# Optimization experiments

Measured on AMD Instinct MI355X. Metric: run time of the kernel, lower is better.

## Reference

```python
import jax, jax.numpy as jnp
from jax import lax
import numpy as np

# inferred ssconv semantics (custom CUDA kernel not in source):
#  - input x: (B, H, W, Cin) channels-last, Cin = per-pixel channel count
#  - in_index: (B, H, W) in [0, IN_GROUPS): routes each input pixel's Cin channels
#    to the corresponding slice of the weight's input-channel dim (gather/scatter MoE-style dispatch)
#  - weight: (OUT_GROUPS*Cout, IN_GROUPS*Cin, kh, kw), bias: (OUT_GROUPS*Cout,)
#  - per output pixel, one out-group is selected (maxout over groups); the kernel
#    returns both the selected Cout channels and the winning group index (out_index)

IN_GROUPS = 4
OUT_GROUPS = 4
STRIDE = 1  # pad = stride//2 in the wrapper; output (H-1)//s+1 == SAME padding


def setup_inputs() -> dict:
    key = jax.random.key(0)
    k1, k2, k3, k4 = jax.random.split(key, 4)
    x = jax.random.normal(k1, (8, 256, 256, 16), dtype=jnp.float32)
    in_index = jax.random.randint(k2, (8, 256, 256), 0, IN_GROUPS, dtype=jnp.int32)
    weight = jax.random.normal(k3, (64, 64, 3, 3), dtype=jnp.float32) * 0.05
    bias = jax.random.normal(k4, (64,), dtype=jnp.float32) * 0.05
    return {"x": x, "in_index": in_index, "weight": weight, "bias": bias}


def reference(x, in_index, weight, bias):
    B, H, W, Cin = x.shape
    OC, IC, kh, kw = weight.shape  # OC = OUT_GROUPS*Cout, IC = IN_GROUPS*Cin
    Cout = OC // OUT_GROUPS

    # dispatch: scatter each pixel's channels into its in-group slice (rest zero)
    onehot = jax.nn.one_hot(in_index, IN_GROUPS, dtype=x.dtype)          # (B,H,W,G)
    x_full = (onehot[..., :, None] * x[..., None, :]).reshape(B, H, W, IN_GROUPS * Cin)

    # dense conv over the dispatched tensor == per-pixel gathered group weights
    w_hwio = jnp.transpose(weight, (2, 3, 1, 0))  # (kh,kw,IC,OC)
    out = lax.conv_general_dilated(
        x_full, w_hwio, window_strides=(STRIDE, STRIDE), padding="SAME",
        dimension_numbers=("NHWC", "HWIO", "NHWC"))
    out = out + bias  # (B,H',W',OC)

    Bo, Ho, Wo, _ = out.shape
    out_g = out.reshape(Bo, Ho, Wo, OUT_GROUPS, Cout)
    scores = out_g.max(axis=-1)                    # (B,H',W',G) per-group response
    out_index = jnp.argmax(scores, axis=-1)        # winning out-group per pixel
    sel = jnp.take_along_axis(out_g, out_index[..., None, None], axis=3)
    sel = jnp.squeeze(sel, axis=3)                 # (B,H',W',Cout)
    return sel, out_index.astype(jnp.int32)
```

## Files before the change

### kernel.cpp

```cpp
#include <hip/hip_runtime.h>

#define H 256
#define W 256
#define BATCH 8
#define CIN 16
#define TW 32
#define TH 4
#define HWC (TW + 2)
#define HHC (TH + 2)
#define NHALO (HWC * HHC)
#define FIX_CAP 16384
#define GAP_TAU 1e-3f

typedef __attribute__((ext_vector_type(8))) short short8;
typedef __attribute__((ext_vector_type(8))) _Float16 half8;
typedef __attribute__((ext_vector_type(4))) float f32x4;

union S8H8 { short8 s; half8 h; };
__device__ __forceinline__ half8 as_h8(short8 s) { S8H8 u; u.s = s; return u.h; }
union HU { _Float16 h; unsigned short u; };
__device__ __forceinline__ unsigned short f2h_bits(float f) { HU u; u.h = (_Float16)f; return u.u; }
__device__ __forceinline__ float h2f(unsigned short b) { HU u; u.u = b; return (float)u.h; }

__device__ __forceinline__ float4 add4(float4 a, float4 b) {
    return make_float4(a.x + b.x, a.y + b.y, a.z + b.z, a.w + b.w);
}
__device__ __forceinline__ float max4(float4 a) {
    return fmaxf(fmaxf(a.x, a.y), fmaxf(a.z, a.w));
}

__global__ void wprep_kernel(const float* __restrict__ w, unsigned short* __restrict__ wt) {
    int i = blockIdx.x * 256 + threadIdx.x;
    if (i >= 73728) return;
    int k   = i & 63;
    int n   = (i >> 6) & 63;
    int sel = (i >> 12) & 1;
    int tap = i >> 13;
    float v = w[(n * 64 + k) * 9 + tap] * 64.0f;
    unsigned short hb = f2h_bits(v);
    unsigned short ob = sel ? f2h_bits((v - h2f(hb)) * 2048.0f) : hb;
    wt[(((tap * 2 + sel) * 64) + n) * 64 + k] = ob;
}

#define CVT(F, VH, VL, J) { unsigned short hb_ = f2h_bits(F); \
    VH[J] = (short)hb_; VL[J] = (short)f2h_bits(((F) - h2f(hb_)) * 2048.0f); }

__global__ __launch_bounds__(256, 2) void ssconv_mfma_kernel(
    const float* __restrict__ x, const int* __restrict__ gidx,
    const unsigned short* __restrict__ wt, const float* __restrict__ bias,
    float* __restrict__ out_sel, float* __restrict__ out_idx,
    unsigned* __restrict__ fix_cnt, unsigned* __restrict__ fix_list)
{
    __shared__ unsigned short hHi[NHALO * 16];
    __shared__ unsigned short hLo[NHALO * 16];
    __shared__ int gsL[NHALO];
    __shared__ __align__(16) unsigned short bufS[17408];

    const int tid = threadIdx.x;
    const int x0 = blockIdx.x * TW;
    const int y0 = blockIdx.y * TH;
    const int bz = blockIdx.z;

    if (tid < NHALO) {
        int r = tid / HWC, c = tid % HWC;
        int hy = y0 + r - 1, hx = x0 + c - 1;
        bool ok = (hy >= 0) && (hy < H) && (hx >= 0) && (hx < W);
        float4 a0 = make_float4(0, 0, 0, 0), a1 = a0, a2 = a0, a3 = a0;
        int g = 0;
        if (ok) {
            const float4* src = (const float4*)(x + (((size_t)bz * H + hy) * W + hx) * CIN);
            a0 = src[0]; a1 = src[1]; a2 = src[2]; a3 = src[3];
            g = gidx[((size_t)bz * H + hy) * W + hx];
        }
        gsL[tid] = g;
        short8 vh0, vl0, vh1, vl1;
        CVT(a0.x, vh0, vl0, 0) CVT(a0.y, vh0, vl0, 1) CVT(a0.z, vh0, vl0, 2) CVT(a0.w, vh0, vl0, 3)
        CVT(a1.x, vh0, vl0, 4) CVT(a1.y, vh0, vl0, 5) CVT(a1.z, vh0, vl0, 6) CVT(a1.w, vh0, vl0, 7)
        CVT(a2.x, vh1, vl1, 0) CVT(a2.y, vh1, vl1, 1) CVT(a2.z, vh1, vl1, 2) CVT(a2.w, vh1, vl1, 3)
        CVT(a3.x, vh1, vl1, 4) CVT(a3.y, vh1, vl1, 5) CVT(a3.z, vh1, vl1, 6) CVT(a3.w, vh1, vl1, 7)
        *(short8*)&hHi[tid * 16 + 0] = vh0;
        *(short8*)&hHi[tid * 16 + 8] = vh1;
        *(short8*)&hLo[tid * 16 + 0] = vl0;
        *(short8*)&hLo[tid * 16 + 8] = vl1;
    }

    const int wvid = tid >> 6;
    const int L    = tid & 63;
    const int q    = L >> 4;
    const int lm   = L & 15;

    {
        const unsigned short* wsrc = wt;
        for (int it = 0; it < 4; ++it) {
            int i = it * 256 + tid;
            int ko = i & 7, n = (i >> 3) & 63, sel = i >> 9;
            short8 v = *(const short8*)(wsrc + (sel * 64 + n) * 64 + ko * 8);
            *(short8*)(bufS + (sel * 64 + n) * 72 + ko * 8) = v;
        }
    }
    __syncthreads();

    f32x4 acc0h[4] = {}, acc1h[4] = {};
    f32x4 acc0l[4] = {}, acc1l[4] = {};

#pragma unroll 1
    for (int tap = 0; tap < 9; ++tap) {
        const int dy = tap / 3, dx = tap % 3;
        const int hb0 = (wvid + dy) * HWC + lm + dx;
        const int hb1 = hb0 + 16;
        const int g0 = gsL[hb0];
        const int g1 = gsL[hb1];

#pragma unroll
        for (int ks = 0; ks < 2; ++ks) {
            const int gk = ks * 2 + (q >> 1);
            const int c0 = (q & 1) * 8;
            short8 z = (short8)0;
            short8 ah0 = *(const short8*)&hHi[hb0 * 16 + c0];
            short8 al0 = *(const short8*)&hLo[hb0 * 16 + c0];
            short8 ah1 = *(const short8*)&hHi[hb1 * 16 + c0];
            short8 al1 = *(const short8*)&hLo[hb1 * 16 + c0];
            bool m0 = (g0 == gk), m1 = (g1 == gk);
            ah0 = m0 ? ah0 : z;  al0 = m0 ? al0 : z;
            ah1 = m1 ? ah1 : z;  al1 = m1 ? al1 : z;

            short8 bh[4];
#pragma unroll
            for (int nt = 0; nt < 4; ++nt)
                bh[nt] = *(const short8*)(bufS + (nt * 16 + lm) * 72 + ks * 32 + q * 8);
#pragma unroll
            for (int nt = 0; nt < 4; ++nt) {
                acc0h[nt] = __builtin_amdgcn_mfma_f32_16x16x32_f16(as_h8(ah0), as_h8(bh[nt]), acc0h[nt], 0, 0, 0);
                acc1h[nt] = __builtin_amdgcn_mfma_f32_16x16x32_f16(as_h8(ah1), as_h8(bh[nt]), acc1h[nt], 0, 0, 0);
                acc0l[nt] = __builtin_amdgcn_mfma_f32_16x16x32_f16(as_h8(al0), as_h8(bh[nt]), acc0l[nt], 0, 0, 0);
                acc1l[nt] = __builtin_amdgcn_mfma_f32_16x16x32_f16(as_h8(al1), as_h8(bh[nt]), acc1l[nt], 0, 0, 0);
            }
#pragma unroll
            for (int nt = 0; nt < 4; ++nt) {
                short8 bl = *(const short8*)(bufS + (64 + nt * 16 + lm) * 72 + ks * 32 + q * 8);
                acc0l[nt] = __builtin_amdgcn_mfma_f32_16x16x32_f16(as_h8(ah0), as_h8(bl), acc0l[nt], 0, 0, 0);
                acc1l[nt] = __builtin_amdgcn_mfma_f32_16x16x32_f16(as_h8(ah1), as_h8(bl), acc1l[nt], 0, 0, 0);
            }
        }
        __syncthreads();
        if (tap < 8) {
            const unsigned short* wsrc = wt + (size_t)(tap + 1) * 8192;
            for (int it = 0; it < 4; ++it) {
                int i = it * 256 + tid;
                int ko = i & 7, n = (i >> 3) & 63, sel = i >> 9;
                short8 v = *(const short8*)(wsrc + (sel * 64 + n) * 64 + ko * 8);
                *(short8*)(bufS + (sel * 64 + n) * 72 + ko * 8) = v;
            }
            __syncthreads();
        }
    }

    const float SH = 0.015625f;
    const float SL = 7.62939453125e-6f;
    float* outS = (float*)bufS;
#pragma unroll
    for (int nt = 0; nt < 4; ++nt) {
#pragma unroll
        for (int r = 0; r < 4; ++r) {
            int xcol0 = q * 4 + r;
            outS[wvid * 2176 + xcol0 * 68 + nt * 16 + lm] =
                acc0h[nt][r] * SH + acc0l[nt][r] * SL;
            outS[wvid * 2176 + (16 + xcol0) * 68 + nt * 16 + lm] =
                acc1h[nt][r] * SH + acc1l[nt][r] * SL;
        }
    }
    __syncthreads();

    {
        int p  = tid >> 1;
        int hh = tid & 1;
        int pw = p >> 5, px_ = p & 31;
        const float4* srcp = (const float4*)(outS + pw * 2176 + px_ * 68 + hh * 32);
        const float4* bb = (const float4*)(bias + hh * 32);
        float4 r0 = add4(srcp[0], bb[0]), r1 = add4(srcp[1], bb[1]);
        float4 r2 = add4(srcp[2], bb[2]), r3 = add4(srcp[3], bb[3]);
        float4 r4 = add4(srcp[4], bb[4]), r5 = add4(srcp[5], bb[5]);
        float4 r6 = add4(srcp[6], bb[6]), r7 = add4(srcp[7], bb[7]);

        float ma = fmaxf(fmaxf(max4(r0), max4(r1)), fmaxf(max4(r2), max4(r3)));
        float mb = fmaxf(fmaxf(max4(r4), max4(r5)), fmaxf(max4(r6), max4(r7)));
        float pa = __shfl_xor(ma, 1, 64);
        float pb = __shfl_xor(mb, 1, 64);
        float s0, s1, s2, s3;
        if (hh == 0) { s0 = ma; s1 = mb; s2 = pa; s3 = pb; }
        else         { s0 = pa; s1 = pb; s2 = ma; s3 = mb; }
        int bg = 0; float best = s0;
        if (s1 > best) { best = s1; bg = 1; }
        if (s2 > best) { best = s2; bg = 2; }
        if (s3 > best) { best = s3; bg = 3; }

        int gy = y0 + pw, gx = x0 + px_;
        size_t opix = ((size_t)bz * H + gy) * W + gx;
        if ((bg >> 1) == hh) {
            bool useB = (bg & 1) != 0;
            float4 o0 = useB ? r4 : r0, o1 = useB ? r5 : r1;
            float4 o2 = useB ? r6 : r2, o3 = useB ? r7 : r3;
            float4* os = (float4*)(out_sel + opix * 16);
            os[0] = o0; os[1] = o1; os[2] = o2; os[3] = o3;
        }
        if (hh == 0) {
            out_idx[opix] = (float)bg;
            float o1v = (bg == 0) ? s1 : s0;
            float o2v = (bg <= 1) ? s2 : s1;
            float o3v = (bg <= 2) ? s3 : s2;
            float second = fmaxf(o1v, fmaxf(o2v, o3v));
            if (best - second < GAP_TAU) {
                unsigned slot = atomicAdd(fix_cnt, 1u);
                if (slot < FIX_CAP) fix_list[slot] = (unsigned)opix;
            }
        }
    }
}

__global__ void fixup_kernel(const float* __restrict__ x, const int* __restrict__ gidx,
                             const float* __restrict__ w, const float* __restrict__ bias,
                             float* __restrict__ out_sel, float* __restrict__ out_idx,
                             const unsigned* __restrict__ fix_cnt,
                             const unsigned* __restrict__ fix_list)
{
    unsigned n = *fix_cnt;
    if (n > FIX_CAP) n = FIX_CAP;
    const int lane = threadIdx.x & 63;
    const int nwaves = gridDim.x * (blockDim.x >> 6);
    unsigned widx = blockIdx.x * (blockDim.x >> 6) + (threadIdx.x >> 6);

    for (; widx < n; widx += nwaves) {
        unsigned opix = fix_list[widx];
        int b  = opix >> 16;
        int y  = (opix >> 8) & 255;
        int xc = opix & 255;
        double acc = (double)bias[lane];
        for (int dy = 0; dy < 3; ++dy) {
            int yy = y + dy - 1;
            if (yy < 0 || yy >= H) continue;
            for (int dx = 0; dx < 3; ++dx) {
                int xx = xc + dx - 1;
                if (xx < 0 || xx >= W) continue;
                size_t pix = ((size_t)b * H + yy) * W + xx;
                int g = gidx[pix];
                const float* xp = x + pix * 16;
                const float* wp = w + (size_t)(lane * 64 + g * 16) * 9 + (dy * 3 + dx);
#pragma unroll
                for (int c = 0; c < 16; ++c)
                    acc = fma((double)wp[c * 9], (double)xp[c], acc);
            }
        }
        double m = acc;
        m = fmax(m, __shfl_xor(m, 1, 64));
        m = fmax(m, __shfl_xor(m, 2, 64));
        m = fmax(m, __shfl_xor(m, 4, 64));
        m = fmax(m, __shfl_xor(m, 8, 64));
        double g0 = __shfl(m, 0, 64), g1 = __shfl(m, 16, 64);
        double g2 = __shfl(m, 32, 64), g3 = __shfl(m, 48, 64);
        int bg = 0; double bb = g0;
        if (g1 > bb) { bb = g1; bg = 1; }
        if (g2 > bb) { bb = g2; bg = 2; }
        if (g3 > bb) { bb = g3; bg = 3; }
        if ((lane >> 4) == bg) out_sel[(size_t)opix * 16 + (lane & 15)] = (float)acc;
        if (lane == 0) out_idx[opix] = (float)bg;
    }
}

extern "C" void kernel_launch(void* const* d_in, const int* in_sizes, int n_in,
                              void* d_out, int out_size, void* d_ws, size_t ws_size,
                              hipStream_t stream) {
    const float* x    = (const float*)d_in[0];
    const int*   gidx = (const int*)d_in[1];
    const float* w    = (const float*)d_in[2];
    const float* bias = (const float*)d_in[3];

    unsigned short* wt = (unsigned short*)d_ws;
    unsigned* fix_cnt  = (unsigned*)((char*)d_ws + 147456);
    unsigned* fix_list = (unsigned*)((char*)d_ws + 147472);

    float* out_sel = (float*)d_out;
    float* out_idx = (float*)d_out + (size_t)BATCH * H * W * CIN;

    hipMemsetAsync(fix_cnt, 0, 16, stream);
    wprep_kernel<<<288, 256, 0, stream>>>(w, wt);

    dim3 grid(W / TW, H / TH, BATCH);
    ssconv_mfma_kernel<<<grid, 256, 0, stream>>>(x, gidx, wt, bias, out_sel, out_idx,
                                                 fix_cnt, fix_list);
    fixup_kernel<<<256, 256, 0, stream>>>(x, gidx, w, bias, out_sel, out_idx,
                                          fix_cnt, fix_list);
}
```

Measured before the change: 210.8 us.

## Drop split-fp16 compensation, double-buffer weights, widen fixup margin

Removes the hi/lo fp16 split for both activations and weights, so the main conv does a single fp16 MFMA pass instead of four-plus products per tile. This cuts MFMA work and LDS footprint, enabling 4 blocks per CU. Weight tiles for the next tap are prefetched into registers and written to a second LDS buffer, removing one barrier per tap. To keep the argmax correct under the lower precision, the near-tie threshold is raised and the exact fp64 fixup reads a transposed weight copy for coalesced access. The fixup falls back to all pixels if the list overflows, and the cap now depends on the workspace size. More pixels will be recomputed in fp64, and output values carry fp16-level error.

Measured after the change: 450.2 us. 2.14x slower.

```diff
diff --git a/kernel.cpp b/kernel.cpp
--- a/kernel.cpp
+++ b/kernel.cpp
@@ -9,8 +9,8 @@
 #define HWC (TW + 2)
 #define HHC (TH + 2)
 #define NHALO (HWC * HHC)
-#define FIX_CAP 16384
-#define GAP_TAU 1e-3f
+#define NPIX_TOTAL (BATCH * H * W)
+#define GAP_TAU 8e-3f
 
 typedef __attribute__((ext_vector_type(8))) short short8;
 typedef __attribute__((ext_vector_type(8))) _Float16 half8;
@@ -20,7 +20,6 @@
 __device__ __forceinline__ half8 as_h8(short8 s) { S8H8 u; u.s = s; return u.h; }
 union HU { _Float16 h; unsigned short u; };
 __device__ __forceinline__ unsigned short f2h_bits(float f) { HU u; u.h = (_Float16)f; return u.u; }
-__device__ __forceinline__ float h2f(unsigned short b) { HU u; u.u = b; return (float)u.h; }
 
 __device__ __forceinline__ float4 add4(float4 a, float4 b) {
     return make_float4(a.x + b.x, a.y + b.y, a.z + b.z, a.w + b.w);
@@ -29,32 +28,28 @@
     return fmaxf(fmaxf(a.x, a.y), fmaxf(a.z, a.w));
 }
 
-__global__ void wprep_kernel(const float* __restrict__ w, unsigned short* __restrict__ wt) {
+__global__ void wprep_kernel(const float* __restrict__ w, unsigned short* __restrict__ wt,
+                             float* __restrict__ wT, unsigned* __restrict__ fix_cnt) {
     int i = blockIdx.x * 256 + threadIdx.x;
-    if (i >= 73728) return;
-    int k   = i & 63;
-    int n   = (i >> 6) & 63;
-    int sel = (i >> 12) & 1;
-    int tap = i >> 13;
-    float v = w[(n * 64 + k) * 9 + tap] * 64.0f;
-    unsigned short hb = f2h_bits(v);
-    unsigned short ob = sel ? f2h_bits((v - h2f(hb)) * 2048.0f) : hb;
-    wt[(((tap * 2 + sel) * 64) + n) * 64 + k] = ob;
-}
-
-#define CVT(F, VH, VL, J) { unsigned short hb_ = f2h_bits(F); \
-    VH[J] = (short)hb_; VL[J] = (short)f2h_bits(((F) - h2f(hb_)) * 2048.0f); }
-
-__global__ __launch_bounds__(256, 2) void ssconv_mfma_kernel(
+    if (blockIdx.x == 0 && threadIdx.x < 4) fix_cnt[threadIdx.x] = 0u;
+    if (i >= 36864) return;
+    int ic  = i & 63;
+    int oc  = (i >> 6) & 63;
+    int tap = i >> 12;
+    float v = w[(oc * 64 + ic) * 9 + tap];
+    wt[(tap * 64 + oc) * 64 + ic] = f2h_bits(v * 64.0f);
+    wT[(tap * 64 + ic) * 64 + oc] = v;
+}
+
+__global__ __launch_bounds__(256, 4) void ssconv_mfma_kernel(
     const float* __restrict__ x, const int* __restrict__ gidx,
     const unsigned short* __restrict__ wt, const float* __restrict__ bias,
     float* __restrict__ out_sel, float* __restrict__ out_idx,
-    unsigned* __restrict__ fix_cnt, unsigned* __restrict__ fix_list)
+    unsigned* __restrict__ fix_cnt, unsigned* __restrict__ fix_list, unsigned fix_cap)
 {
     __shared__ unsigned short hHi[NHALO * 16];
-    __shared__ unsigned short hLo[NHALO * 16];
     __shared__ int gsL[NHALO];
-    __shared__ __align__(16) unsigned short bufS[17408];
+    __shared__ __align__(16) unsigned short bufS[9216];
 
     const int tid = threadIdx.x;
     const int x0 = blockIdx.x * TW;
@@ -73,15 +68,17 @@
             g = gidx[((size_t)bz * H + hy) * W + hx];
         }
         gsL[tid] = g;
-        short8 vh0, vl0, vh1, vl1;
-        CVT(a0.x, vh0, vl0, 0) CVT(a0.y, vh0, vl0, 1) CVT(a0.z, vh0, vl0, 2) CVT(a0.w, vh0, vl0, 3)
-        CVT(a1.x, vh0, vl0, 4) CVT(a1.y, vh0, vl0, 5) CVT(a1.z, vh0, vl0, 6) CVT(a1.w, vh0, vl0, 7)
-        CVT(a2.x, vh1, vl1, 0) CVT(a2.y, vh1, vl1, 1) CVT(a2.z, vh1, vl1, 2) CVT(a2.w, vh1, vl1, 3)
-        CVT(a3.x, vh1, vl1, 4) CVT(a3.y, vh1, vl1, 5) CVT(a3.z, vh1, vl1, 6) CVT(a3.w, vh1, vl1, 7)
-        *(short8*)&hHi[tid * 16 + 0] = vh0;
-        *(short8*)&hHi[tid * 16 + 8] = vh1;
-        *(short8*)&hLo[tid * 16 + 0] = vl0;
-        *(short8*)&hLo[tid * 16 + 8] = vl1;
+        short8 v0, v1;
+        v0[0] = (short)f2h_bits(a0.x); v0[1] = (short)f2h_bits(a0.y);
+        v0[2] = (short)f2h_bits(a0.z); v0[3] = (short)f2h_bits(a0.w);
+        v0[4] = (short)f2h_bits(a1.x); v0[5] = (short)f2h_bits(a1.y);
+        v0[6] = (short)f2h_bits(a1.z); v0[7] = (short)f2h_bits(a1.w);
+        v1[0] = (short)f2h_bits(a2.x); v1[1] = (short)f2h_bits(a2.y);
+        v1[2] = (short)f2h_bits(a2.z); v1[3] = (short)f2h_bits(a2.w);
+        v1[4] = (short)f2h_bits(a3.x); v1[5] = (short)f2h_bits(a3.y);
+        v1[6] = (short)f2h_bits(a3.z); v1[7] = (short)f2h_bits(a3.w);
+        *(short8*)&hHi[tid * 16 + 0] = v0;
+        *(short8*)&hHi[tid * 16 + 8] = v1;
     }
 
     const int wvid = tid >> 6;
@@ -89,22 +86,33 @@
     const int q    = L >> 4;
     const int lm   = L & 15;
 
+    unsigned short* bufA = bufS;
+    unsigned short* bufB = bufS + 4608;
+
     {
-        const unsigned short* wsrc = wt;
-        for (int it = 0; it < 4; ++it) {
-            int i = it * 256 + tid;
-            int ko = i & 7, n = (i >> 3) & 63, sel = i >> 9;
-            short8 v = *(const short8*)(wsrc + (sel * 64 + n) * 64 + ko * 8);
-            *(short8*)(bufS + (sel * 64 + n) * 72 + ko * 8) = v;
-        }
+        int i0 = tid, i1 = 256 + tid;
+        short8 v0 = *(const short8*)(wt + (i0 >> 3) * 64 + (i0 & 7) * 8);
+        short8 v1 = *(const short8*)(wt + (i1 >> 3) * 64 + (i1 & 7) * 8);
+        *(short8*)(bufA + (i0 >> 3) * 72 + (i0 & 7) * 8) = v0;
+        *(short8*)(bufA + (i1 >> 3) * 72 + (i1 & 7) * 8) = v1;
     }
     __syncthreads();
 
-    f32x4 acc0h[4] = {}, acc1h[4] = {};
-    f32x4 acc0l[4] = {}, acc1l[4] = {};
+    f32x4 acc0[4] = {}, acc1[4] = {};
 
 #pragma unroll 1
     for (int tap = 0; tap < 9; ++tap) {
+        unsigned short* cur = (tap & 1) ? bufB : bufA;
+        unsigned short* nxt = (tap & 1) ? bufA : bufB;
+
+        short8 p0, p1;
+        if (tap < 8) {
+            const unsigned short* wsrc = wt + (size_t)(tap + 1) * 4096;
+            int i0 = tid, i1 = 256 + tid;
+            p0 = *(const short8*)(wsrc + (i0 >> 3) * 64 + (i0 & 7) * 8);
+            p1 = *(const short8*)(wsrc + (i1 >> 3) * 64 + (i1 & 7) * 8);
+        }
+
         const int dy = tap / 3, dx = tap % 3;
         const int hb0 = (wvid + dy) * HWC + lm + dx;
         const int hb1 = hb0 + 16;
@@ -117,120 +125,103 @@
             const int c0 = (q & 1) * 8;
             short8 z = (short8)0;
             short8 ah0 = *(const short8*)&hHi[hb0 * 16 + c0];
-            short8 al0 = *(const short8*)&hLo[hb0 * 16 + c0];
             short8 ah1 = *(const short8*)&hHi[hb1 * 16 + c0];
-            short8 al1 = *(const short8*)&hLo[hb1 * 16 + c0];
-            bool m0 = (g0 == gk), m1 = (g1 == gk);
-            ah0 = m0 ? ah0 : z;  al0 = m0 ? al0 : z;
-            ah1 = m1 ? ah1 : z;  al1 = m1 ? al1 : z;
+            ah0 = (g0 == gk) ? ah0 : z;
+            ah1 = (g1 == gk) ? ah1 : z;
 
             short8 bh[4];
 #pragma unroll
             for (int nt = 0; nt < 4; ++nt)
-                bh[nt] = *(const short8*)(bufS + (nt * 16 + lm) * 72 + ks * 32 + q * 8);
+                bh[nt] = *(const short8*)(cur + (nt * 16 + lm) * 72 + ks * 32 + q * 8);
 #pragma unroll
             for (int nt = 0; nt < 4; ++nt) {
-                acc0h[nt] = __builtin_amdgcn_mfma_f32_16x16x32_f16(as_h8(ah0), as_h8(bh[nt]), acc0h[nt], 0, 0, 0);
-                acc1h[nt] = __builtin_amdgcn_mfma_f32_16x16x32_f16(as_h8(ah1), as_h8(bh[nt]), acc1h[nt], 0, 0, 0);
-                acc0l[nt] = __builtin_amdgcn_mfma_f32_16x16x32_f16(as_h8(al0), as_h8(bh[nt]), acc0l[nt], 0, 0, 0);
-                acc1l[nt] = __builtin_amdgcn_mfma_f32_16x16x32_f16(as_h8(al1), as_h8(bh[nt]), acc1l[nt], 0, 0, 0);
-            }
-#pragma unroll
-            for (int nt = 0; nt < 4; ++nt) {
-                short8 bl = *(const short8*)(bufS + (64 + nt * 16 + lm) * 72 + ks * 32 + q * 8);
-                acc0l[nt] = __builtin_amdgcn_mfma_f32_16x16x32_f16(as_h8(ah0), as_h8(bl), acc0l[nt], 0, 0, 0);
-                acc1l[nt] = __builtin_amdgcn_mfma_f32_16x16x32_f16(as_h8(ah1), as_h8(bl), acc1l[nt], 0, 0, 0);
-            }
+                acc0[nt] = __builtin_amdgcn_mfma_f32_16x16x32_f16(as_h8(ah0), as_h8(bh[nt]), acc0[nt], 0, 0, 0);
+                acc1[nt] = __builtin_amdgcn_mfma_f32_16x16x32_f16(as_h8(ah1), as_h8(bh[nt]), acc1[nt], 0, 0, 0);
+            }
+        }
+
+        if (tap < 8) {
+            int i0 = tid, i1 = 256 + tid;
+            *(short8*)(nxt + (i0 >> 3) * 72 + (i0 & 7) * 8) = p0;
+            *(short8*)(nxt + (i1 >> 3) * 72 + (i1 & 7) * 8) = p1;
         }
         __syncthreads();
-        if (tap < 8) {
-            const unsigned short* wsrc = wt + (size_t)(tap + 1) * 8192;
-            for (int it = 0; it < 4; ++it) {
-                int i = it * 256 + tid;
-                int ko = i & 7, n = (i >> 3) & 63, sel = i >> 9;
-                short8 v = *(const short8*)(wsrc + (sel * 64 + n) * 64 + ko * 8);
-                *(short8*)(bufS + (sel * 64 + n) * 72 + ko * 8) = v;
-            }
-            __syncthreads();
-        }
     }
 
     const float SH = 0.015625f;
-    const float SL = 7.62939453125e-6f;
     float* outS = (float*)bufS;
-#pragma unroll
-    for (int nt = 0; nt < 4; ++nt) {
-#pragma unroll
-        for (int r = 0; r < 4; ++r) {
-            int xcol0 = q * 4 + r;
-            outS[wvid * 2176 + xcol0 * 68 + nt * 16 + lm] =
-                acc0h[nt][r] * SH + acc0l[nt][r] * SL;
-            outS[wvid * 2176 + (16 + xcol0) * 68 + nt * 16 + lm] =
-                acc1h[nt][r] * SH + acc1l[nt][r] * SL;
-        }
-    }
-    __syncthreads();
-
-    {
-        int p  = tid >> 1;
-        int hh = tid & 1;
-        int pw = p >> 5, px_ = p & 31;
-        const float4* srcp = (const float4*)(outS + pw * 2176 + px_ * 68 + hh * 32);
-        const float4* bb = (const float4*)(bias + hh * 32);
+
+#pragma unroll 1
+    for (int mt = 0; mt < 2; ++mt) {
+        if (mt) __syncthreads();
+        f32x4* am = mt ? acc1 : acc0;
+#pragma unroll
+        for (int nt = 0; nt < 4; ++nt) {
+#pragma unroll
+            for (int r = 0; r < 4; ++r) {
+                outS[wvid * 1088 + (q * 4 + r) * 68 + nt * 16 + lm] = am[nt][r] * SH;
+            }
+        }
+        __syncthreads();
+
+        int p  = tid >> 2;
+        int hh = tid & 3;
+        int pw = p >> 4, px16 = p & 15;
+        const float4* srcp = (const float4*)(outS + pw * 1088 + px16 * 68 + hh * 16);
+        const float4* bb = (const float4*)(bias + hh * 16);
         float4 r0 = add4(srcp[0], bb[0]), r1 = add4(srcp[1], bb[1]);
         float4 r2 = add4(srcp[2], bb[2]), r3 = add4(srcp[3], bb[3]);
-        float4 r4 = add4(srcp[4], bb[4]), r5 = add4(srcp[5], bb[5]);
-        float4 r6 = add4(srcp[6], bb[6]), r7 = add4(srcp[7], bb[7]);
-
-        float ma = fmaxf(fmaxf(max4(r0), max4(r1)), fmaxf(max4(r2), max4(r3)));
-        float mb = fmaxf(fmaxf(max4(r4), max4(r5)), fmaxf(max4(r6), max4(r7)));
-        float pa = __shfl_xor(ma, 1, 64);
-        float pb = __shfl_xor(mb, 1, 64);
-        float s0, s1, s2, s3;
-        if (hh == 0) { s0 = ma; s1 = mb; s2 = pa; s3 = pb; }
-        else         { s0 = pa; s1 = pb; s2 = ma; s3 = mb; }
-        int bg = 0; float best = s0;
-        if (s1 > best) { best = s1; bg = 1; }
-        if (s2 > best) { best = s2; bg = 2; }
-        if (s3 > best) { best = s3; bg = 3; }
-
-        int gy = y0 + pw, gx = x0 + px_;
+
+        float m  = fmaxf(fmaxf(max4(r0), max4(r1)), fmaxf(max4(r2), max4(r3)));
+        float v1 = __shfl_xor(m, 1, 64);
+        float v2 = __shfl_xor(m, 2, 64);
+        float v3 = __shfl_xor(m, 3, 64);
+
+        float g0 = (hh == 0) ? m  : (hh == 1) ? v1 : (hh == 2) ? v2 : v3;
+        float g1 = (hh == 0) ? v1 : (hh == 1) ? m  : (hh == 2) ? v3 : v2;
+        float g2 = (hh == 0) ? v2 : (hh == 1) ? v3 : (hh == 2) ? m  : v1;
+        float g3 = (hh == 0) ? v3 : (hh == 1) ? v2 : (hh == 2) ? v1 : m;
+
+        int bg = 0; float best = g0;
+        if (g1 > best) { best = g1; bg = 1; }
+        if (g2 > best) { best = g2; bg = 2; }
+        if (g3 > best) { best = g3; bg = 3; }
+
+        int gy = y0 + pw, gx = x0 + mt * 16 + px16;
         size_t opix = ((size_t)bz * H + gy) * W + gx;
-        if ((bg >> 1) == hh) {
-            bool useB = (bg & 1) != 0;
-            float4 o0 = useB ? r4 : r0, o1 = useB ? r5 : r1;
-            float4 o2 = useB ? r6 : r2, o3 = useB ? r7 : r3;
+        if (hh == bg) {
             float4* os = (float4*)(out_sel + opix * 16);
-            os[0] = o0; os[1] = o1; os[2] = o2; os[3] = o3;
+            os[0] = r0; os[1] = r1; os[2] = r2; os[3] = r3;
         }
         if (hh == 0) {
             out_idx[opix] = (float)bg;
-            float o1v = (bg == 0) ? s1 : s0;
-            float o2v = (bg <= 1) ? s2 : s1;
-            float o3v = (bg <= 2) ? s3 : s2;
-            float second = fmaxf(o1v, fmaxf(o2v, o3v));
-            if (best - second < GAP_TAU) {
+            float o1 = (bg == 0) ? fmaxf(g1, fmaxf(g2, g3))
+                     : (bg == 1) ? fmaxf(g0, fmaxf(g2, g3))
+                     : (bg == 2) ? fmaxf(g0, fmaxf(g1, g3))
+                                 : fmaxf(g0, fmaxf(g1, g2));
+            if (best - o1 < GAP_TAU) {
                 unsigned slot = atomicAdd(fix_cnt, 1u);
-                if (slot < FIX_CAP) fix_list[slot] = (unsigned)opix;
+                if (slot < fix_cap) fix_list[slot] = (unsigned)opix;
             }
         }
     }
 }
 
 __global__ void fixup_kernel(const float* __restrict__ x, const int* __restrict__ gidx,
-                             const float* __restrict__ w, const float* __restrict__ bias,
+                             const float* __restrict__ wT, const float* __restrict__ bias,
                              float* __restrict__ out_sel, float* __restrict__ out_idx,
                              const unsigned* __restrict__ fix_cnt,
-                             const unsigned* __restrict__ fix_list)
+                             const unsigned* __restrict__ fix_list, unsigned fix_cap)
 {
     unsigned n = *fix_cnt;
-    if (n > FIX_CAP) n = FIX_CAP;
+    const bool full = (n > fix_cap);
+    const unsigned total = full ? (unsigned)NPIX_TOTAL : n;
     const int lane = threadIdx.x & 63;
-    const int nwaves = gridDim.x * (blockDim.x >> 6);
+    const unsigned nwaves = gridDim.x * (blockDim.x >> 6);
     unsigned widx = blockIdx.x * (blockDim.x >> 6) + (threadIdx.x >> 6);
 
-    for (; widx < n; widx += nwaves) {
-        unsigned opix = fix_list[widx];
+    for (; widx < total; widx += nwaves) {
+        unsigned opix = full ? widx : fix_list[widx];
         int b  = opix >> 16;
         int y  = (opix >> 8) & 255;
         int xc = opix & 255;
@@ -244,10 +235,10 @@
                 size_t pix = ((size_t)b * H + yy) * W + xx;
                 int g = gidx[pix];
                 const float* xp = x + pix * 16;
-                const float* wp = w + (size_t)(lane * 64 + g * 16) * 9 + (dy * 3 + dx);
+                const float* wp = wT + (size_t)((dy * 3 + dx) * 64 + g * 16) * 64 + lane;
 #pragma unroll
                 for (int c = 0; c < 16; ++c)
-                    acc = fma((double)wp[c * 9], (double)xp[c], acc);
+                    acc = fma((double)wp[c * 64], (double)xp[c], acc);
             }
         }
         double m = acc;
@@ -275,18 +266,21 @@
     const float* bias = (const float*)d_in[3];
 
     unsigned short* wt = (unsigned short*)d_ws;
-    unsigned* fix_cnt  = (unsigned*)((char*)d_ws + 147456);
-    unsigned* fix_list = (unsigned*)((char*)d_ws + 147472);
+    float* wT          = (float*)((char*)d_ws + 73728);
+    unsigned* fix_cnt  = (unsigned*)((char*)d_ws + 221184);
+    unsigned* fix_list = (unsigned*)((char*)d_ws + 221200);
+
+    size_t avail = (ws_size > 221200) ? (ws_size - 221200) / 4 : 0;
+    unsigned fix_cap = (unsigned)(avail < (size_t)NPIX_TOTAL ? avail : (size_t)NPIX_TOTAL);
 
     float* out_sel = (float*)d_out;
     float* out_idx = (float*)d_out + (size_t)BATCH * H * W * CIN;
 
-    hipMemsetAsync(fix_cnt, 0, 16, stream);
-    wprep_kernel<<<288, 256, 0, stream>>>(w, wt);
+    wprep_kernel<<<144, 256, 0, stream>>>(w, wt, wT, fix_cnt);
 
     dim3 grid(W / TW, H / TH, BATCH);
     ssconv_mfma_kernel<<<grid, 256, 0, stream>>>(x, gidx, wt, bias, out_sel, out_idx,
-                                                 fix_cnt, fix_list);
-    fixup_kernel<<<256, 256, 0, stream>>>(x, gidx, w, bias, out_sel, out_idx,
-                                          fix_cnt, fix_list);
-}
+                                                 fix_cnt, fix_list, fix_cap);
+    fixup_kernel<<<1024, 256, 0, stream>>>(x, gidx, wT, bias, out_sel, out_idx,
+                                           fix_cnt, fix_list, fix_cap);
+}
```
